# Performance work log

Measured on AMD Instinct MI355X. Metric: run time of the kernel, lower is better.

Reference implementation:

```python
import jax, jax.numpy as jnp
import numpy as np

B, T, V, E, L, H = 128, 512, 128, 64, 128, 512  # batch, seq, vocab, char_emb, latent, hidden


def setup_inputs() -> dict:
    key = jax.random.key(0)
    ks = jax.random.split(key, 12)
    r = lambda k, shape, s=0.05: jax.random.normal(k, shape, dtype=jnp.float32) * s
    return {
        "char_ids": jax.random.randint(ks[0], (B, T), 0, V),
        "z": jax.random.normal(ks[1], (B, L), dtype=jnp.float32),
        "emb": r(ks[2], (V, E)),
        "cw1": r(ks[3], (L, H)), "cb1": jnp.zeros((H,)), "cg1": jnp.ones((H,)), "cbeta1": jnp.zeros((H,)),
        "cw2": r(ks[4], (H, H)), "cb2": jnp.zeros((H,)), "cg2": jnp.ones((H,)), "cbeta2": jnp.zeros((H,)),
        "wih0": r(ks[5], (4 * H, E + H + 2)), "whh0": r(ks[6], (4 * H, H)),
        "bih0": jnp.zeros((4 * H,)), "bhh0": jnp.zeros((4 * H,)),
        "wih1": r(ks[7], (4 * H, H)), "whh1": r(ks[8], (4 * H, H)),
        "bih1": jnp.zeros((4 * H,)), "bhh1": jnp.zeros((4 * H,)),
        "wo1": r(ks[9], (H, H // 2)), "bo1": jnp.zeros((H // 2,)),
        "wo2": r(ks[10], (H // 2, 2)), "bo2": jnp.zeros((2,)),
        "init_timing": jnp.zeros((2,)),
    }


def _ln(x, g, b, eps=1e-5):
    m = jnp.mean(x, -1, keepdims=True)
    v = jnp.var(x, -1, keepdims=True)
    return (x - m) * jax.lax.rsqrt(v + eps) * g + b


def _lstm_cell(x, h, c, wih, whh, bih, bhh):
    # PyTorch gate order: i, f, g, o
    gates = x @ wih.T + bih + h @ whh.T + bhh
    i, f, g, o = jnp.split(gates, 4, axis=-1)
    c = jax.nn.sigmoid(f) * c + jax.nn.sigmoid(i) * jnp.tanh(g)
    h = jax.nn.sigmoid(o) * jnp.tanh(c)
    return h, c


def reference(char_ids, z, emb, cw1, cb1, cg1, cbeta1, cw2, cb2, cg2, cbeta2,
              wih0, whh0, bih0, bhh0, wih1, whh1, bih1, bhh1,
              wo1, bo1, wo2, bo2, init_timing):
    b = char_ids.shape[0]
    # condition encoder: Linear -> LN -> LeakyReLU(0.2), twice
    cond = jax.nn.leaky_relu(_ln(z @ cw1 + cb1, cg1, cbeta1), 0.2)
    cond = jax.nn.leaky_relu(_ln(cond @ cw2 + cb2, cg2, cbeta2), 0.2)  # (B, H)
    xs = jnp.transpose(emb[char_ids], (1, 0, 2))  # (T, B, E)
    h0 = jnp.zeros((b, H), jnp.float32)
    c0 = jnp.zeros((b, H), jnp.float32)
    h1 = jnp.zeros((b, H), jnp.float32)
    c1 = jnp.zeros((b, H), jnp.float32)
    prev = jnp.broadcast_to(init_timing, (b, 2))

    def step(carry, xt):
        h0, c0, h1, c1, prev = carry
        xin = jnp.concatenate([xt, cond, prev], axis=-1)  # (B, E+H+2)
        h0, c0 = _lstm_cell(xin, h0, c0, wih0, whh0, bih0, bhh0)
        h1, c1 = _lstm_cell(h0, h1, c1, wih1, whh1, bih1, bhh1)
        out = jax.nn.leaky_relu(h1 @ wo1 + bo1, 0.2) @ wo2 + bo2
        out = jax.nn.softplus(out) + 0.005  # (B, 2)
        return (h0, c0, h1, c1, out), out

    _, ys = jax.lax.scan(step, (h0, c0, h1, c1, prev), xs)
    return jnp.transpose(ys, (1, 0, 2))  # (B, T, 2)
```

## Files before the change

kernel.cpp:

```cpp
#include <hip/hip_runtime.h>

#define Bn 128
#define Tn 512
#define Vn 128
#define En 64
#define Ln 128
#define Hn 512
#define G4 2048
#define WGS 256
#define NTHR 512
#define NALL (WGS * NTHR)
#define LSTR 520
#define GRPS 8
#define WPG 32
#define RPG 16

typedef unsigned short u16;
typedef unsigned int u32;
typedef __bf16 bf16x8 __attribute__((ext_vector_type(8)));
typedef float f32x4 __attribute__((ext_vector_type(4)));
typedef u32 u32x4 __attribute__((ext_vector_type(4)));

__device__ inline float bf2f(u16 h) {
    u32 u = ((u32)h) << 16;
    float f;
    __builtin_memcpy(&f, &u, 4);
    return f;
}
__device__ inline u16 f2bf(float f) {
    u32 u;
    __builtin_memcpy(&u, &f, 4);
    u32 r = (u + 0x7fffu + ((u >> 16) & 1u)) >> 16;
    return (u16)r;
}
__device__ inline u32 f2u(float f) { u32 u; __builtin_memcpy(&u, &f, 4); return u; }
__device__ inline float u2f(u32 u) { float f; __builtin_memcpy(&f, &u, 4); return f; }
__device__ inline float sigm(float x) { return 1.f / (1.f + expf(-x)); }
__device__ inline float leaky(float x) { return x > 0.f ? x : 0.2f * x; }
__device__ inline float softplus(float x) {
    return x > 0.f ? x + log1pf(expf(-x)) : log1pf(expf(x));
}

__device__ inline void cload16(const u32* p, u32* w) {
    u32x4 v0, v1, v2, v3;
    asm volatile(
        "global_load_dwordx4 %0, %4, off sc0 sc1\n\t"
        "global_load_dwordx4 %1, %4, off offset:16 sc0 sc1\n\t"
        "global_load_dwordx4 %2, %4, off offset:32 sc0 sc1\n\t"
        "global_load_dwordx4 %3, %4, off offset:48 sc0 sc1\n\t"
        "s_waitcnt vmcnt(0)"
        : "=&v"(v0), "=&v"(v1), "=&v"(v2), "=&v"(v3)
        : "v"(p)
        : "memory");
    *(u32x4*)(w) = v0;
    *(u32x4*)(w + 4) = v1;
    *(u32x4*)(w + 8) = v2;
    *(u32x4*)(w + 12) = v3;
}
__device__ inline u32 cload1(const u32* p) {
    u32 v;
    asm volatile("global_load_dword %0, %1, off sc0 sc1\n\ts_waitcnt vmcnt(0)"
                 : "=v"(v) : "v"(p) : "memory");
    return v;
}
__device__ inline void cwait() { asm volatile("s_waitcnt vmcnt(0)" ::: "memory"); }
__device__ inline void cstore1(u32* p, u32 v) {
    asm volatile("global_store_dword %0, %1, off sc0 sc1" :: "v"(p), "v"(v) : "memory");
}

#define OFF_FLAGS  0x000000
#define OFF_B1SUM  0x002000
#define OFF_WP     0x004000
#define OFF_BIAS0  0x008000
#define OFF_CPAR   0x00A000
#define OFF_H0P    0x010000
#define OFF_H1P    0x050000
#define OFF_PART   0x090000
#define OFF_WO1TH  0x0B0000
#define OFF_WO1TL  0x0F0000
#define OFF_ZF     0x130000
#define OFF_CW1F   0x140000
#define OFF_CW2F   0x180000
#define OFF_CONDF  0x280000
#define OFF_YBUF   0x2C0000
#define OFF_BASE0  0x300000
#define OFF_EMBW   0x400000
#define OFF_W0HI   0x500000
#define OFF_W0LO   0x700000
#define OFF_W1HI   0x900000
#define OFF_W1LO   0xB00000
#define OFF_WI1HI  0xD00000
#define OFF_WI1LO  0xF00000

__device__ inline void gbar_heavy(int* cnt, int* gen) {
    __syncthreads();
    if (threadIdx.x == 0) {
        __threadfence();
        int g = __hip_atomic_load(gen, __ATOMIC_RELAXED, __HIP_MEMORY_SCOPE_AGENT);
        int arrived = __hip_atomic_fetch_add(cnt, 1, __ATOMIC_ACQ_REL, __HIP_MEMORY_SCOPE_AGENT);
        if (arrived == WGS - 1) {
            __hip_atomic_store(cnt, 0, __ATOMIC_RELAXED, __HIP_MEMORY_SCOPE_AGENT);
            __hip_atomic_store(gen, g + 1, __ATOMIC_RELEASE, __HIP_MEMORY_SCOPE_AGENT);
        } else {
            while (__hip_atomic_load(gen, __ATOMIC_ACQUIRE, __HIP_MEMORY_SCOPE_AGENT) == g)
                __builtin_amdgcn_s_sleep(1);
        }
        __threadfence();
    }
    __syncthreads();
}

__device__ inline void poll32(const u32* gf, u32 sq) {
    const int l = threadIdx.x & 31;
    for (;;) {
        u32 v = cload1(gf + l);
        if (__all((int)(v >= sq))) break;
        __builtin_amdgcn_s_sleep(4);
    }
}
__device__ inline void poll16(const u32* gf, u32 sq) {
    const int l = threadIdx.x & 15;
    for (;;) {
        u32 v = cload1(gf + l);
        if (__all((int)(v >= sq))) break;
        __builtin_amdgcn_s_sleep(4);
    }
}

__device__ inline void unpack16(const u32* w, u16* ph, u16* pl) {
    u32 hd[8], ld[8];
#pragma unroll
    for (int i = 0; i < 8; ++i) {
        hd[i] = (w[2 * i] & 0xFFFFu) | (w[2 * i + 1] << 16);
        ld[i] = (w[2 * i] >> 16) | (w[2 * i + 1] & 0xFFFF0000u);
    }
    *(u32x4*)(ph) = *(const u32x4*)(hd);
    *(u32x4*)(ph + 8) = *(const u32x4*)(hd + 4);
    *(u32x4*)(pl) = *(const u32x4*)(ld);
    *(u32x4*)(pl + 8) = *(const u32x4*)(ld + 4);
}

#define MF(a, b, c) __builtin_amdgcn_mfma_f32_16x16x32_bf16(a, b, c, 0, 0, 0)

__device__ inline f32x4 gemm16_3(const u16* __restrict__ Ah, const u16* __restrict__ Al,
                                 const u16* __restrict__ Bhb, const u16* __restrict__ Blb,
                                 int colb, int n, int q) {
    const u16* Bh = Bhb + (size_t)(colb + n) * Hn;
    const u16* Bl = Blb + (size_t)(colb + n) * Hn;
    const int a0 = n * LSTR;
    f32x4 c0 = {0.f, 0.f, 0.f, 0.f}, c1 = c0, c2 = c0;
#pragma unroll 4
    for (int it = 0; it < 16; ++it) {
        const int ko = it * 32 + q * 8;
        bf16x8 bh = *(const bf16x8*)(Bh + ko);
        bf16x8 bl = *(const bf16x8*)(Bl + ko);
        bf16x8 ah = *(const bf16x8*)(Ah + a0 + ko);
        bf16x8 al = *(const bf16x8*)(Al + a0 + ko);
        c0 = MF(ah, bh, c0);
        c1 = MF(al, bh, c1);
        c2 = MF(ah, bl, c2);
    }
    return c0 + c1 + c2;
}

__device__ inline f32x4 gemm16_regB3(const u16* __restrict__ Ah, const u16* __restrict__ Al,
                                     const bf16x8* wa, const bf16x8* wb, int n, int q) {
    const int a0 = n * LSTR;
    f32x4 c0 = {0.f, 0.f, 0.f, 0.f}, c1 = c0, c2 = c0;
#pragma unroll
    for (int it = 0; it < 16; ++it) {
        const int ko = it * 32 + q * 8;
        bf16x8 ah = *(const bf16x8*)(Ah + a0 + ko);
        bf16x8 al = *(const bf16x8*)(Al + a0 + ko);
        c0 = MF(ah, wa[it], c0);
        c1 = MF(al, wa[it], c1);
        c2 = MF(ah, wb[it], c2);
    }
    return c0 + c1 + c2;
}

__device__ inline f32x4 gemm16_regB2(const u16* __restrict__ Ah, const u16* __restrict__ Al,
                                     const bf16x8* wb, int n, int q) {
    const int a0 = n * LSTR;
    f32x4 c0 = {0.f, 0.f, 0.f, 0.f}, c1 = c0;
#pragma unroll
    for (int it = 0; it < 16; ++it) {
        const int ko = it * 32 + q * 8;
        bf16x8 ah = *(const bf16x8*)(Ah + a0 + ko);
        bf16x8 al = *(const bf16x8*)(Al + a0 + ko);
        c0 = MF(ah, wb[it], c0);
        c1 = MF(al, wb[it], c1);
    }
    return c0 + c1;
}

__device__ inline f32x4 gemm16_ldsB3(const u16* __restrict__ Ah, const u16* __restrict__ Al,
                                     const u16* __restrict__ Bh, const u16* __restrict__ Bl,
                                     int n, int q) {
    const int a0 = n * LSTR;
    f32x4 c0 = {0.f, 0.f, 0.f, 0.f}, c1 = c0, c2 = c0;
#pragma unroll 4
    for (int it = 0; it < 16; ++it) {
        const int ko = it * 32 + q * 8;
        bf16x8 bh = *(const bf16x8*)(Bh + a0 + ko);
        bf16x8 bl = *(const bf16x8*)(Bl + a0 + ko);
        bf16x8 ah = *(const bf16x8*)(Ah + a0 + ko);
        bf16x8 al = *(const bf16x8*)(Al + a0 + ko);
        c0 = MF(ah, bh, c0);
        c1 = MF(al, bh, c1);
        c2 = MF(ah, bl, c2);
    }
    return c0 + c1 + c2;
}

__device__ inline void stage(float* dst, const void* src, int n, int gtid, bool isbf) {
    if (isbf) {
        const u16* s = (const u16*)src;
        for (int e = gtid; e < n; e += NALL) dst[e] = bf2f(s[e]);
    } else {
        const float* s = (const float*)src;
        for (int e = gtid; e < n; e += NALL) dst[e] = s[e];
    }
}
__device__ inline void stage_split(u16* hi, u16* lo, const void* src, int n, int gtid, bool isbf) {
    if (isbf) {
        const u16* s = (const u16*)src;
        for (int e = gtid; e < n; e += NALL) { hi[e] = s[e]; lo[e] = 0; }
    } else {
        const float* s = (const float*)src;
        for (int e = gtid; e < n; e += NALL) {
            float w = s[e];
            u16 h = f2bf(w);
            hi[e] = h;
            lo[e] = f2bf(w - bf2f(h));
        }
    }
}

template <bool ISBF>
__device__ inline float ldw(const void* p, size_t i) {
    if constexpr (ISBF) return bf2f(((const u16*)p)[i]);
    else return ((const float*)p)[i];
}

template <bool ISBF>
__device__ void phase5(const void* wih0, const void* emb, const float* __restrict__ condf,
                       const float* __restrict__ bias0f, float* __restrict__ base0,
                       float* __restrict__ embW, int gtid) {
    const int cc = gtid & 2047;
    const int bb0 = gtid >> 11;
    float b = bias0f[cc];
    float a0 = b, a1 = b, a2 = b, a3 = b;
    const float* c0p = condf + (size_t)bb0 * Hn;
    const float* c1p = condf + (size_t)(bb0 + 32) * Hn;
    const float* c2p = condf + (size_t)(bb0 + 64) * Hn;
    const float* c3p = condf + (size_t)(bb0 + 96) * Hn;
    const size_t wb = (size_t)cc * 578 + 64;
    for (int k = 0; k < Hn; ++k) {
        float w = ldw<ISBF>(wih0, wb + k);
        a0 += c0p[k] * w; a1 += c1p[k] * w; a2 += c2p[k] * w; a3 += c3p[k] * w;
    }
    base0[(size_t)bb0 * G4 + cc] = a0;
    base0[(size_t)(bb0 + 32) * G4 + cc] = a1;
    base0[(size_t)(bb0 + 64) * G4 + cc] = a2;
    base0[(size_t)(bb0 + 96) * G4 + cc] = a3;
    float e0 = 0.f, e1 = 0.f, e2 = 0.f, e3 = 0.f;
    const size_t wb2 = (size_t)cc * 578;
    for (int k = 0; k < En; ++k) {
        float w = ldw<ISBF>(wih0, wb2 + k);
        e0 += ldw<ISBF>(emb, (size_t)bb0 * En + k) * w;
        e1 += ldw<ISBF>(emb, (size_t)(bb0 + 32) * En + k) * w;
        e2 += ldw<ISBF>(emb, (size_t)(bb0 + 64) * En + k) * w;
        e3 += ldw<ISBF>(emb, (size_t)(bb0 + 96) * En + k) * w;
    }
    embW[(size_t)bb0 * G4 + cc] = e0;
    embW[(size_t)(bb0 + 32) * G4 + cc] = e1;
    embW[(size_t)(bb0 + 64) * G4 + cc] = e2;
    embW[(size_t)(bb0 + 96) * G4 + cc] = e3;
}

__device__ inline void ln_leaky_row(const float* __restrict__ x, const float* __restrict__ gamma,
                                    const float* __restrict__ beta, float* __restrict__ out,
                                    float* red) {
    int tid = threadIdx.x;
    float v = x[tid];
    float s = v, s2 = v * v;
    for (int off = 32; off; off >>= 1) {
        s += __shfl_down(s, off);
        s2 += __shfl_down(s2, off);
    }
    int wv = tid >> 6;
    if ((tid & 63) == 0) { red[wv * 2] = s; red[wv * 2 + 1] = s2; }
    __syncthreads();
    if (tid == 0) {
        float ts = 0.f, ts2 = 0.f;
        for (int i = 0; i < 8; ++i) { ts += red[i * 2]; ts2 += red[i * 2 + 1]; }
        float m = ts / 512.f;
        float var = ts2 / 512.f - m * m;
        red[16] = m;
        red[17] = rsqrtf(var + 1e-5f);
    }
    __syncthreads();
    float m = red[16], rs = red[17];
    out[tid] = leaky((v - m) * rs * gamma[tid] + beta[tid]);
    __syncthreads();
}

__global__ void init_flags_kernel(int* flags) { flags[threadIdx.x] = 0; }

__global__ __launch_bounds__(NTHR, 2) void gen_kernel(
    const int* __restrict__ char_ids, const void* z, const void* emb,
    const void* cw1, const void* cb1, const void* cg1, const void* cbeta1,
    const void* cw2, const void* cb2, const void* cg2, const void* cbeta2,
    const void* wih0, const void* whh0, const void* bih0, const void* bhh0,
    const void* wih1, const void* whh1, const void* bih1, const void* bhh1,
    const void* wo1, const void* bo1, const void* wo2, const void* bo2,
    const void* init_t, void* outp, char* __restrict__ ws) {
    __shared__ u16 lh0h[RPG * LSTR];
    __shared__ u16 lh0l[RPG * LSTR];
    __shared__ u16 lh1h[RPG * LSTR];
    __shared__ u16 lh1l[RPG * LSTR];
    __shared__ u16 lwoh[16 * LSTR];
    __shared__ u16 lwol[16 * LSTR];
    __shared__ float smemx[1024];
    __shared__ float pvs[32];
    __shared__ float red[34];

    int* flags = (int*)(ws + OFF_FLAGS);
    float* b1sum = (float*)(ws + OFF_B1SUM);
    float* wpb = (float*)(ws + OFF_WP);
    float* bias0f = (float*)(ws + OFF_BIAS0);
    float* cpar = (float*)(ws + OFF_CPAR);
    u32* h0p = (u32*)(ws + OFF_H0P);
    u32* h1p = (u32*)(ws + OFF_H1P);
    float* partf = (float*)(ws + OFF_PART);
    u16* wo1Th = (u16*)(ws + OFF_WO1TH);
    u16* wo1Tl = (u16*)(ws + OFF_WO1TL);
    float* zf = (float*)(ws + OFF_ZF);
    float* cw1f = (float*)(ws + OFF_CW1F);
    float* cw2f = (float*)(ws + OFF_CW2F);
    float* condf = (float*)(ws + OFF_CONDF);
    float* ybuf = (float*)(ws + OFF_YBUF);
    float* base0 = (float*)(ws + OFF_BASE0);
    float* embW = (float*)(ws + OFF_EMBW);
    u16* W0hi = (u16*)(ws + OFF_W0HI);
    u16* W0lo = (u16*)(ws + OFF_W0LO);
    u16* W1hi = (u16*)(ws + OFF_W1HI);
    u16* W1lo = (u16*)(ws + OFF_W1LO);
    u16* Wi1hi = (u16*)(ws + OFF_WI1HI);
    u16* Wi1lo = (u16*)(ws + OFF_WI1LO);
    float* wo1f = base0;

    const bool isbf = (((const u32*)cg1)[0] == 0x3F803F80u);

    const int g = blockIdx.x;
    const int tid = threadIdx.x;
    const int wv = tid >> 6;
    const int grp = g & 7;
    const int ut = g >> 3;
    const int mat = wv >> 2;
    const int gw = wv & 3;
    const int R0g = grp * RPG;
    const int colb = gw * 512 + ut * 16;
    const int lane = tid & 63;
    const int n = lane & 15;
    const int q = lane >> 4;
    const int gtid = g * NTHR + tid;
    const f32x4 Z4 = {0.f, 0.f, 0.f, 0.f};

    u32* gf = (u32*)flags + grp * 64;
    u32* gf2 = (u32*)flags + grp * 64 + 32;
    u32* gfl = gf + ut;
    int* hcnt = flags + 512;
    int* hgen = flags + 528;
    float* part = partf + grp * 1024;

    stage_split(W0hi, W0lo, whh0, G4 * Hn, gtid, isbf);
    stage_split(W1hi, W1lo, whh1, G4 * Hn, gtid, isbf);
    stage_split(Wi1hi, Wi1lo, wih1, G4 * Hn, gtid, isbf);
    stage(zf, z, Bn * Ln, gtid, isbf);
    stage(cw1f, cw1, Ln * Hn, gtid, isbf);
    stage(cw2f, cw2, Hn * Hn, gtid, isbf);
    stage(cpar + 0, cg1, 512, gtid, isbf);
    stage(cpar + 512, cbeta1, 512, gtid, isbf);
    stage(cpar + 1024, cg2, 512, gtid, isbf);
    stage(cpar + 1536, cbeta2, 512, gtid, isbf);
    stage(cpar + 2048, bo1, 256, gtid, isbf);
    stage(cpar + 2304, bo2, 2, gtid, isbf);
    stage(cpar + 2560, cb2, 512, gtid, isbf);
    stage(cpar + 3072, cb1, 512, gtid, isbf);
    stage(cpar + 3584, wo2, 256 * 2, gtid, isbf);
    stage(wo1f, wo1, Hn * 256, gtid, isbf);
    if (gtid < Bn * Hn) { cstore1(h0p + gtid, 0); cstore1(h1p + gtid, 0); }
    if (isbf) {
        if (gtid < G4) b1sum[gtid] = bf2f(((const u16*)bih1)[gtid]) + bf2f(((const u16*)bhh1)[gtid]);
        if (gtid < G4) bias0f[gtid] = bf2f(((const u16*)bih0)[gtid]) + bf2f(((const u16*)bhh0)[gtid]);
        if (gtid < 4096) {
            size_t ix = (size_t)(gtid >> 1) * 578 + 576 + (gtid & 1);
            wpb[gtid] = bf2f(((const u16*)wih0)[ix]);
        }
    } else {
        if (gtid < G4) b1sum[gtid] = ((const float*)bih1)[gtid] + ((const float*)bhh1)[gtid];
        if (gtid < G4) bias0f[gtid] = ((const float*)bih0)[gtid] + ((const float*)bhh0)[gtid];
        if (gtid < 4096) {
            size_t ix = (size_t)(gtid >> 1) * 578 + 576 + (gtid & 1);
            wpb[gtid] = ((const float*)wih0)[ix];
        }
    }
    gbar_heavy(hcnt, hgen);
    if (gtid < Bn * Hn) {
        int bb = gtid >> 9, nn = gtid & 511;
        float a = cpar[3072 + nn];
        const float* zr = zf + bb * Ln;
        for (int k = 0; k < Ln; ++k) a += zr[k] * cw1f[k * Hn + nn];
        ybuf[gtid] = a;
    }
    for (int e = gtid; e < 256 * Hn; e += NALL) {
        int nn = e >> 9, kk = e & 511;
        float w = wo1f[kk * 256 + nn];
        u16 hv = f2bf(w);
        wo1Th[e] = hv;
        wo1Tl[e] = f2bf(w - bf2f(hv));
    }
    gbar_heavy(hcnt, hgen);
    if (g < Bn) ln_leaky_row(ybuf + g * Hn, cpar + 0, cpar + 512, condf + g * Hn, red);
    gbar_heavy(hcnt, hgen);
    if (g < Bn) {
        float a = cpar[2560 + tid];
        const float* crow = condf + g * Hn;
        for (int k = 0; k < Hn; ++k) a += crow[k] * cw2f[k * Hn + tid];
        ybuf[g * Hn + tid] = a;
    }
    gbar_heavy(hcnt, hgen);
    if (g < Bn) ln_leaky_row(ybuf + g * Hn, cpar + 1024, cpar + 1536, condf + g * Hn, red);
    gbar_heavy(hcnt, hgen);
    if (gtid < Bn * Hn) {
        if (isbf) phase5<true>(wih0, emb, condf, bias0f, base0, embW, gtid);
        else phase5<false>(wih0, emb, condf, bias0f, base0, embW, gtid);
    }
    gbar_heavy(hcnt, hgen);

    const bool headwg = (ut < 16);
    bf16x8 wA[16], wB[16];
    {
        const u16* BhA = (mat == 0 ? W0hi : W1hi) + (size_t)(colb + n) * Hn;
        const u16* BhB;
        if (isbf) {
            if (mat == 1) BhB = Wi1hi + (size_t)(colb + n) * Hn;
            else if (headwg && wv == 0) BhB = wo1Th + (size_t)(ut * 16 + n) * Hn;
            else BhB = BhA;
        } else {
            BhB = (mat == 0 ? W0lo : W1lo) + (size_t)(colb + n) * Hn;
        }
#pragma unroll
        for (int it = 0; it < 16; ++it) {
            wA[it] = *(const bf16x8*)(BhA + it * 32 + q * 8);
            wB[it] = *(const bf16x8*)(BhB + it * 32 + q * 8);
        }
    }
    if (!isbf && headwg) {
        for (int e = tid; e < 16 * Hn; e += NTHR) {
            int col = e >> 9, k = e & 511;
            lwoh[col * LSTR + k] = wo1Th[(size_t)(ut * 16 + col) * Hn + k];
            lwol[col * LSTR + k] = wo1Tl[(size_t)(ut * 16 + col) * Hn + k];
        }
    }

    float c0 = 0.f, c1 = 0.f;
    const int lr = tid >> 4;
    const int un = tid & 15;
    const int bb = R0g + lr;
    const int uu = ut * 16 + un;
    const float* bo1f = cpar + 2048;
    const float* bo2f = cpar + 2304;
    const float* wo2f = cpar + 3584;
    const int srow = tid >> 5;
    const int blk = tid & 31;
    const int kub = blk * 16;
    f32x4 acc1c = Z4;

    for (int e = tid; e < RPG * LSTR; e += NTHR) {
        lh0h[e] = 0; lh0l[e] = 0; lh1h[e] = 0; lh1l[e] = 0;
    }
    if (tid < 32) pvs[tid] = isbf ? bf2f(((const u16*)init_t)[tid & 1])
                                  : ((const float*)init_t)[tid & 1];

    for (int t = 0; t < Tn; ++t) {
        if (t >= 1) {
            if (wv == 0) poll32(gf, 2 * (u32)t);
            __syncthreads();
            if (blk != ut) {
                u32 w[16];
                cload16(h1p + (size_t)(R0g + srow) * Hn + kub, w);
                unpack16(w, lh1h + srow * LSTR + kub, lh1l + srow * LSTR + kub);
            }
        }
        __syncthreads();
        if (headwg && wv == 0 && t >= 1) {
            f32x4 ha = isbf ? gemm16_regB2(lh1h, lh1l, wB, n, q)
                            : gemm16_ldsB3(lh1h, lh1l, lwoh, lwol, n, q);
            float p[4][2];
#pragma unroll
            for (int r = 0; r < 4; ++r) {
                float hv = leaky(ha[r] + bo1f[ut * 16 + n]);
                p[r][0] = hv * wo2f[(ut * 16 + n) * 2];
                p[r][1] = hv * wo2f[(ut * 16 + n) * 2 + 1];
            }
#pragma unroll
            for (int r = 0; r < 4; ++r)
#pragma unroll
                for (int j = 0; j < 2; ++j) {
                    float s = p[r][j];
                    s += __shfl_xor(s, 1, 16);
                    s += __shfl_xor(s, 2, 16);
                    s += __shfl_xor(s, 4, 16);
                    s += __shfl_xor(s, 8, 16);
                    p[r][j] = s;
                }
            if (n == 0) {
#pragma unroll
                for (int r = 0; r < 4; ++r)
#pragma unroll
                    for (int j = 0; j < 2; ++j) {
                        int row = q * 4 + r;
                        cstore1((u32*)(part + (row * 2 + j) * 16 + ut), f2u(p[r][j]));
                    }
            }
            cwait();
            if (tid == 0) cstore1(gf2 + ut, (u32)t);
        }
        if (mat == 0) {
            f32x4 a = isbf ? gemm16_regB2(lh0h, lh0l, wA, n, q)
                           : gemm16_regB3(lh0h, lh0l, wA, wB, n, q);
#pragma unroll
            for (int r = 0; r < 4; ++r)
                smemx[gw * 256 + (q * 4 + r) * 16 + n] = a[r];
        } else {
            acc1c = isbf ? gemm16_regB2(lh1h, lh1l, wA, n, q)
                         : gemm16_regB3(lh1h, lh1l, wA, wB, n, q);
        }
        if (t >= 1 && wv == 4) {
            poll16(gf2, (u32)t);
            if (tid < 288) {
                int l = tid - 256;
                int row = l >> 1, j = l & 1;
                u32 hw[16];
                cload16((const u32*)(part + (row * 2 + j) * 16), hw);
                float s = bo2f[j];
#pragma unroll
                for (int i = 0; i < 16; ++i) s += u2f(hw[i]);
                float y = softplus(s) + 0.005f;
                pvs[row * 2 + j] = y;
                if (ut == 0) {
                    size_t oi = ((size_t)(R0g + row) * Tn + (t - 1)) * 2 + j;
                    if (isbf) ((u16*)outp)[oi] = f2bf(y);
                    else ((float*)outp)[oi] = y;
                }
            }
        }
        __syncthreads();
        if (tid < 256) {
            int id = char_ids[bb * Tn + t];
            float pv0 = pvs[lr * 2], pv1 = pvs[lr * 2 + 1];
            float gv[4];
#pragma unroll
            for (int gi = 0; gi < 4; ++gi) {
                int cc = gi * 512 + uu;
                gv[gi] = smemx[gi * 256 + lr * 16 + un] + base0[(size_t)bb * G4 + cc] +
                         embW[(size_t)id * G4 + cc] + pv0 * wpb[2 * cc] + pv1 * wpb[2 * cc + 1];
            }
            float ig = sigm(gv[0]), fg = sigm(gv[1]), gg = tanhf(gv[2]), og = sigm(gv[3]);
            c0 = fg * c0 + ig * gg;
            float h = og * tanhf(c0);
            u16 hv = f2bf(h);
            u16 lv = f2bf(h - bf2f(hv));
            lh0h[lr * LSTR + uu] = hv;
            lh0l[lr * LSTR + uu] = lv;
            cstore1(h0p + (size_t)bb * Hn + uu, (u32)hv | ((u32)lv << 16));
        }
        cwait();
        __syncthreads();
        if (tid == 0) cstore1(gfl, 2 * (u32)t + 1);

        if (wv == 0) poll32(gf, 2 * (u32)t + 1);
        __syncthreads();
        if (blk != ut) {
            u32 w[16];
            cload16(h0p + (size_t)(R0g + srow) * Hn + kub, w);
            unpack16(w, lh0h + srow * LSTR + kub, lh0l + srow * LSTR + kub);
        }
        __syncthreads();
        if (mat == 1) {
            f32x4 a = isbf ? gemm16_regB2(lh0h, lh0l, wB, n, q)
                           : gemm16_3(lh0h, lh0l, Wi1hi, Wi1lo, colb, n, q);
            acc1c = acc1c + a;
#pragma unroll
            for (int r = 0; r < 4; ++r)
                smemx[gw * 256 + (q * 4 + r) * 16 + n] = acc1c[r];
        }
        __syncthreads();
        if (tid < 256) {
            float gv[4];
#pragma unroll
            for (int gi = 0; gi < 4; ++gi) {
                int cc = gi * 512 + uu;
                gv[gi] = smemx[gi * 256 + lr * 16 + un] + b1sum[cc];
            }
            float ig = sigm(gv[0]), fg = sigm(gv[1]), gg = tanhf(gv[2]), og = sigm(gv[3]);
            c1 = fg * c1 + ig * gg;
            float h = og * tanhf(c1);
            u16 hv = f2bf(h);
            u16 lv = f2bf(h - bf2f(hv));
            lh1h[lr * LSTR + uu] = hv;
            lh1l[lr * LSTR + uu] = lv;
            cstore1(h1p + (size_t)bb * Hn + uu, (u32)hv | ((u32)lv << 16));
        }
        cwait();
        __syncthreads();
        if (tid == 0) cstore1(gfl, 2 * (u32)t + 2);
    }

    if (wv == 0) poll32(gf, 2 * (u32)Tn);
    __syncthreads();
    if (blk != ut) {
        u32 w[16];
        cload16(h1p + (size_t)(R0g + srow) * Hn + kub, w);
        unpack16(w, lh1h + srow * LSTR + kub, lh1l + srow * LSTR + kub);
    }
    __syncthreads();
    if (headwg && wv == 0) {
        f32x4 ha = isbf ? gemm16_regB2(lh1h, lh1l, wB, n, q)
                        : gemm16_ldsB3(lh1h, lh1l, lwoh, lwol, n, q);
        float p[4][2];
#pragma unroll
        for (int r = 0; r < 4; ++r) {
            float hv = leaky(ha[r] + bo1f[ut * 16 + n]);
            p[r][0] = hv * wo2f[(ut * 16 + n) * 2];
            p[r][1] = hv * wo2f[(ut * 16 + n) * 2 + 1];
        }
#pragma unroll
        for (int r = 0; r < 4; ++r)
#pragma unroll
            for (int j = 0; j < 2; ++j) {
                float s = p[r][j];
                s += __shfl_xor(s, 1, 16);
                s += __shfl_xor(s, 2, 16);
                s += __shfl_xor(s, 4, 16);
                s += __shfl_xor(s, 8, 16);
                p[r][j] = s;
            }
        if (n == 0) {
#pragma unroll
            for (int r = 0; r < 4; ++r)
#pragma unroll
                for (int j = 0; j < 2; ++j) {
                    int row = q * 4 + r;
                    cstore1((u32*)(part + (row * 2 + j) * 16 + ut), f2u(p[r][j]));
                }
        }
        cwait();
        if (tid == 0) cstore1(gf2 + ut, (u32)Tn);
    }
    if (ut == 0 && wv == 0) {
        poll16(gf2, (u32)Tn);
        if (tid < 32) {
            int row = tid >> 1, j = tid & 1;
            u32 hw[16];
            cload16((const u32*)(part + (row * 2 + j) * 16), hw);
            float s = bo2f[j];
#pragma unroll
            for (int i = 0; i < 16; ++i) s += u2f(hw[i]);
            float y = softplus(s) + 0.005f;
            size_t oi = ((size_t)(R0g + row) * Tn + (Tn - 1)) * 2 + j;
            if (isbf) ((u16*)outp)[oi] = f2bf(y);
            else ((float*)outp)[oi] = y;
        }
    }
}

extern "C" void kernel_launch(void* const* d_in, const int* in_sizes, int n_in,
                              void* d_out, int out_size, void* d_ws, size_t ws_size,
                              hipStream_t stream) {
    (void)in_sizes; (void)n_in; (void)out_size; (void)ws_size;
    init_flags_kernel<<<1, 1024, 0, stream>>>((int*)d_ws);
    gen_kernel<<<WGS, NTHR, 0, stream>>>(
        (const int*)d_in[0], d_in[1], d_in[2], d_in[3], d_in[4], d_in[5], d_in[6], d_in[7],
        d_in[8], d_in[9], d_in[10], d_in[11], d_in[12], d_in[13], d_in[14], d_in[15], d_in[16],
        d_in[17], d_in[18], d_in[19], d_in[20], d_in[21], d_in[22], d_in[23],
        d_out, (char*)d_ws);
}
```

Measured before the change: 10.19 ms.

## Hoist layer-0 recurrent GEMM before poll and preload loop-invariant gate terms

The layer-0 h·Whh GEMM is moved to the top of each timestep, ahead of the wait on the layer-1 flag, so it overlaps the inter-workgroup sync. Bias, timing weights and embedding rows are loaded into registers once or prefetched early instead of being read from global memory inside the gate math. Workgroup-to-group mapping changes so a group's 32 workgroups are contiguous, the poll sleep is shortened, polling moves to another wave, and the bf16 layer-1 input GEMM now streams weights from global memory instead of holding them in registers. Register pressure rises, and the wB register path for the bf16 case is no longer used there.

```diff
diff --git a/kernel.cpp b/kernel.cpp
--- a/kernel.cpp
+++ b/kernel.cpp
@@ -115,7 +115,7 @@
     for (;;) {
         u32 v = cload1(gf + l);
         if (__all((int)(v >= sq))) break;
-        __builtin_amdgcn_s_sleep(4);
+        __builtin_amdgcn_s_sleep(2);
     }
 }
 __device__ inline void poll16(const u32* gf, u32 sq) {
@@ -123,7 +123,7 @@
     for (;;) {
         u32 v = cload1(gf + l);
         if (__all((int)(v >= sq))) break;
-        __builtin_amdgcn_s_sleep(4);
+        __builtin_amdgcn_s_sleep(2);
     }
 }
 
@@ -161,6 +161,23 @@
         c2 = MF(ah, bl, c2);
     }
     return c0 + c1 + c2;
+}
+
+__device__ inline f32x4 gemm16_s2(const u16* __restrict__ Ah, const u16* __restrict__ Al,
+                                  const u16* __restrict__ Bhb, int colb, int n, int q) {
+    const u16* Bh = Bhb + (size_t)(colb + n) * Hn;
+    const int a0 = n * LSTR;
+    f32x4 c0 = {0.f, 0.f, 0.f, 0.f}, c1 = c0;
+#pragma unroll 4
+    for (int it = 0; it < 16; ++it) {
+        const int ko = it * 32 + q * 8;
+        bf16x8 bh = *(const bf16x8*)(Bh + ko);
+        bf16x8 ah = *(const bf16x8*)(Ah + a0 + ko);
+        bf16x8 al = *(const bf16x8*)(Al + a0 + ko);
+        c0 = MF(ah, bh, c0);
+        c1 = MF(al, bh, c1);
+    }
+    return c0 + c1;
 }
 
 __device__ inline f32x4 gemm16_regB3(const u16* __restrict__ Ah, const u16* __restrict__ Al,
@@ -356,8 +373,8 @@
     const int g = blockIdx.x;
     const int tid = threadIdx.x;
     const int wv = tid >> 6;
-    const int grp = g & 7;
-    const int ut = g >> 3;
+    const int grp = g >> 5;
+    const int ut = g & 31;
     const int mat = wv >> 2;
     const int gw = wv & 3;
     const int R0g = grp * RPG;
@@ -485,9 +502,35 @@
     if (tid < 32) pvs[tid] = isbf ? bf2f(((const u16*)init_t)[tid & 1])
                                   : ((const float*)init_t)[tid & 1];
 
+    float b0v[4], wpv[8], b1v[4];
+    if (tid < 256) {
+#pragma unroll
+        for (int gi = 0; gi < 4; ++gi) {
+            int cc = gi * 512 + uu;
+            b0v[gi] = base0[(size_t)bb * G4 + cc];
+            wpv[2 * gi] = wpb[2 * cc];
+            wpv[2 * gi + 1] = wpb[2 * cc + 1];
+            b1v[gi] = b1sum[cc];
+        }
+    }
+    __syncthreads();
+
     for (int t = 0; t < Tn; ++t) {
+        if (mat == 0) {
+            f32x4 a = isbf ? gemm16_regB2(lh0h, lh0l, wA, n, q)
+                           : gemm16_regB3(lh0h, lh0l, wA, wB, n, q);
+#pragma unroll
+            for (int r = 0; r < 4; ++r)
+                smemx[gw * 256 + (q * 4 + r) * 16 + n] = a[r];
+        }
+        float ew0, ew1, ew2, ew3;
+        if (tid < 256) {
+            int id = char_ids[bb * Tn + t];
+            const float* er = embW + (size_t)id * G4 + uu;
+            ew0 = er[0]; ew1 = er[512]; ew2 = er[1024]; ew3 = er[1536];
+        }
         if (t >= 1) {
-            if (wv == 0) poll32(gf, 2 * (u32)t);
+            if (wv == 7) poll32(gf, 2 * (u32)t);
             __syncthreads();
             if (blk != ut) {
                 u32 w[16];
@@ -529,19 +572,13 @@
             cwait();
             if (tid == 0) cstore1(gf2 + ut, (u32)t);
         }
-        if (mat == 0) {
-            f32x4 a = isbf ? gemm16_regB2(lh0h, lh0l, wA, n, q)
-                           : gemm16_regB3(lh0h, lh0l, wA, wB, n, q);
-#pragma unroll
-            for (int r = 0; r < 4; ++r)
-                smemx[gw * 256 + (q * 4 + r) * 16 + n] = a[r];
-        } else {
+        if (mat == 1) {
             acc1c = isbf ? gemm16_regB2(lh1h, lh1l, wA, n, q)
                          : gemm16_regB3(lh1h, lh1l, wA, wB, n, q);
         }
         if (t >= 1 && wv == 4) {
             poll16(gf2, (u32)t);
-            if (tid < 288) {
+            if (lane < 32) {
                 int l = tid - 256;
                 int row = l >> 1, j = l & 1;
                 u32 hw[16];
@@ -560,15 +597,12 @@
         }
         __syncthreads();
         if (tid < 256) {
-            int id = char_ids[bb * Tn + t];
             float pv0 = pvs[lr * 2], pv1 = pvs[lr * 2 + 1];
             float gv[4];
-#pragma unroll
-            for (int gi = 0; gi < 4; ++gi) {
-                int cc = gi * 512 + uu;
-                gv[gi] = smemx[gi * 256 + lr * 16 + un] + base0[(size_t)bb * G4 + cc] +
-                         embW[(size_t)id * G4 + cc] + pv0 * wpb[2 * cc] + pv1 * wpb[2 * cc + 1];
-            }
+            gv[0] = smemx[0 * 256 + lr * 16 + un] + b0v[0] + ew0 + pv0 * wpv[0] + pv1 * wpv[1];
+            gv[1] = smemx[1 * 256 + lr * 16 + un] + b0v[1] + ew1 + pv0 * wpv[2] + pv1 * wpv[3];
+            gv[2] = smemx[2 * 256 + lr * 16 + un] + b0v[2] + ew2 + pv0 * wpv[4] + pv1 * wpv[5];
+            gv[3] = smemx[3 * 256 + lr * 16 + un] + b0v[3] + ew3 + pv0 * wpv[6] + pv1 * wpv[7];
             float ig = sigm(gv[0]), fg = sigm(gv[1]), gg = tanhf(gv[2]), og = sigm(gv[3]);
             c0 = fg * c0 + ig * gg;
             float h = og * tanhf(c0);
@@ -591,7 +625,7 @@
         }
         __syncthreads();
         if (mat == 1) {
-            f32x4 a = isbf ? gemm16_regB2(lh0h, lh0l, wB, n, q)
+            f32x4 a = isbf ? gemm16_s2(lh0h, lh0l, Wi1hi, colb, n, q)
                            : gemm16_3(lh0h, lh0l, Wi1hi, Wi1lo, colb, n, q);
             acc1c = acc1c + a;
 #pragma unroll
@@ -602,10 +636,8 @@
         if (tid < 256) {
             float gv[4];
 #pragma unroll
-            for (int gi = 0; gi < 4; ++gi) {
-                int cc = gi * 512 + uu;
-                gv[gi] = smemx[gi * 256 + lr * 16 + un] + b1sum[cc];
-            }
+            for (int gi = 0; gi < 4; ++gi)
+                gv[gi] = smemx[gi * 256 + lr * 16 + un] + b1v[gi];
             float ig = sigm(gv[0]), fg = sigm(gv[1]), gg = tanhf(gv[2]), og = sigm(gv[3]);
             c1 = fg * c1 + ig * gg;
             float h = og * tanhf(c1);
```

After: 8.653 ms, median of 2. 15.1% less time.
